# Optimization experiments

Hardware: AMD Instinct MI355X
Metric: run time of the kernel (lower is better)

## Reference

```python
import jax, jax.numpy as jnp
import numpy as np

B, S, H, NH, PF, L = 2, 2048, 1024, 16, 4096, 6
HD = H // NH
EPS = 1e-5


def setup_inputs() -> dict:
    key = jax.random.key(0)
    ks = jax.random.split(key, 12)
    s = lambda k, shp, fan: jax.random.normal(k, shp, jnp.float32) * (1.0 / np.sqrt(fan))
    return {
        "input_tensor": jax.random.normal(ks[0], (B, S, H), jnp.float32),
        "pos_emb": s(ks[1], (S, H), H),
        "Wq": s(ks[2], (L, H, H), H), "bq": jnp.zeros((L, H), jnp.float32),
        "Wk": s(ks[3], (L, H, H), H), "bk": jnp.zeros((L, H), jnp.float32),
        "Wv": s(ks[4], (L, H, H), H), "bv": jnp.zeros((L, H), jnp.float32),
        "Wo": s(ks[5], (L, H, H), H), "bo": jnp.zeros((L, H), jnp.float32),
        "ln_g": jnp.ones((L, H), jnp.float32), "ln_b": jnp.zeros((L, H), jnp.float32),
        "W1": s(ks[6], (L, H, PF), H), "b1": jnp.zeros((L, PF), jnp.float32),
        "W2": s(ks[7], (L, PF, H), PF), "b2": jnp.zeros((L, H), jnp.float32),
    }


def _layernorm(x, g, b):
    mu = jnp.mean(x, axis=-1, keepdims=True)
    var = jnp.mean(jnp.square(x - mu), axis=-1, keepdims=True)
    return (x - mu) * jax.lax.rsqrt(var + EPS) * g + b


def _encoder(input_tensor, pos_emb, params):
    # pos embed: same positions for every batch row
    src = input_tensor * jnp.sqrt(jnp.float32(H)) + pos_emb[None, :, :]

    def layer(src, p):
        Wq, bq, Wk, bk, Wv, bv, Wo, bo, g, b, W1, b1, W2, b2 = p
        q = (src @ Wq + bq).reshape(B, S, NH, HD)
        k = (src @ Wk + bk).reshape(B, S, NH, HD)
        v = (src @ Wv + bv).reshape(B, S, NH, HD)
        # scores [B, NH, S, S]
        energy = jnp.einsum("bqhd,bkhd->bhqk", q, k) / jnp.sqrt(jnp.float32(HD))
        attn = jax.nn.softmax(energy, axis=-1)
        ctx = jnp.einsum("bhqk,bkhd->bqhd", attn, v).reshape(B, S, H)
        attn_out = ctx @ Wo + bo
        src = _layernorm(src + attn_out, g, b)
        ffn = jax.nn.relu(src @ W1 + b1) @ W2 + b2
        src = _layernorm(src + ffn, g, b)  # same LayerNorm reused, as in source
        return src, None

    src, _ = jax.lax.scan(layer, src, params)
    return src


def reference(input_tensor, pos_emb, Wq, bq, Wk, bk, Wv, bv, Wo, bo, ln_g, ln_b, W1, b1, W2, b2):
    params = (Wq, bq, Wk, bk, Wv, bv, Wo, bo, ln_g, ln_b, W1, b1, W2, b2)
    return _encoder(input_tensor, pos_emb, params)
```

## Files before the change

kernel.cpp:

```cpp
#include <hip/hip_runtime.h>
#include <cstdint>

constexpr int Bc = 2, Sc = 2048, Hc = 1024, NHc = 16, HDc = 64, PFc = 4096, Lc = 6;
constexpr float EPSc = 1e-5f;
constexpr float QSC = 0.18033688011112042f;

using f32x4  = __attribute__((ext_vector_type(4))) float;
using bf16x8 = __attribute__((ext_vector_type(8))) __bf16;
using bf16x4 = __attribute__((ext_vector_type(4))) __bf16;
using u32x4  = __attribute__((ext_vector_type(4))) unsigned;

#if __has_builtin(__builtin_amdgcn_exp2f)
#define EXP2(x) __builtin_amdgcn_exp2f(x)
#else
#define EXP2(x) exp2f(x)
#endif

__device__ __forceinline__ f32x4 mfma16(bf16x8 a, bf16x8 b, f32x4 c) {
    return __builtin_amdgcn_mfma_f32_16x16x32_bf16(a, b, c, 0, 0, 0);
}

__device__ __forceinline__ void gload_lds16(const void* g, void* l) {
    __builtin_amdgcn_global_load_lds(
        (__attribute__((address_space(1))) void*)(uintptr_t)g,
        (__attribute__((address_space(3))) void*)(uint32_t)(uintptr_t)l,
        16, 0, 0);
}

struct HL { __bf16 h, l; };
__device__ __forceinline__ HL split2(float v) {
    HL r;
    r.h = (__bf16)v;
    r.l = (__bf16)(v - (float)r.h);
    return r;
}

__device__ __forceinline__ unsigned bfbits(__bf16 x) {
    return (unsigned)__builtin_bit_cast(unsigned short, x);
}
__device__ __forceinline__ unsigned packbf(float a, float b) {
    return bfbits((__bf16)a) | (bfbits((__bf16)b) << 16);
}

__global__ __launch_bounds__(256) void wconv_kernel(
    const float* __restrict__ in, __bf16* __restrict__ out, int K, int N)
{
    __shared__ float tile[64][65];
    const int t = threadIdx.x;
    const size_t lstride = (size_t)K * N;
    const float* ip = in + (size_t)blockIdx.z * lstride;
    __bf16* op = out + (size_t)blockIdx.z * lstride;
    const int n0 = blockIdx.x * 64, k0 = blockIdx.y * 64;
    #pragma unroll
    for (int c = 0; c < 4; ++c) {
        int idx = c * 256 + t;
        int row = idx >> 4;
        int c4  = idx & 15;
        float4 v = *(const float4*)(ip + (size_t)(k0 + row) * N + n0 + c4 * 4);
        tile[row][c4 * 4 + 0] = v.x; tile[row][c4 * 4 + 1] = v.y;
        tile[row][c4 * 4 + 2] = v.z; tile[row][c4 * 4 + 3] = v.w;
    }
    __syncthreads();
    #pragma unroll
    for (int c = 0; c < 4; ++c) {
        int idx = c * 256 + t;
        int n  = idx >> 4;
        int k4 = idx & 15;
        bf16x4 hh = { (__bf16)tile[k4 * 4 + 0][n], (__bf16)tile[k4 * 4 + 1][n],
                      (__bf16)tile[k4 * 4 + 2][n], (__bf16)tile[k4 * 4 + 3][n] };
        *(bf16x4*)(op + (size_t)(n0 + n) * K + k0 + k4 * 4) = hh;
    }
}

__global__ __launch_bounds__(256) void embed_kernel(
    const float* __restrict__ in, const float* __restrict__ pos,
    float* __restrict__ sf, __bf16* __restrict__ sh, __bf16* __restrict__ sl)
{
    const int n4 = (Bc * Sc * Hc) / 4;
    const int pmask = (Sc * Hc / 4) - 1;
    for (int i = blockIdx.x * 256 + threadIdx.x; i < n4; i += gridDim.x * 256) {
        float4 a = ((const float4*)in)[i];
        float4 p = ((const float4*)pos)[i & pmask];
        float4 r;
        r.x = a.x * 32.f + p.x; r.y = a.y * 32.f + p.y;
        r.z = a.z * 32.f + p.z; r.w = a.w * 32.f + p.w;
        ((float4*)sf)[i] = r;
        HL e0 = split2(r.x), e1 = split2(r.y), e2 = split2(r.z), e3 = split2(r.w);
        bf16x4 hh = { e0.h, e1.h, e2.h, e3.h };
        bf16x4 ll = { e0.l, e1.l, e2.l, e3.l };
        ((bf16x4*)sh)[i] = hh;
        ((bf16x4*)sl)[i] = ll;
    }
}

template<int BM, int OUTMODE, bool RELU>
__global__ __launch_bounds__(256) void gemm_bt_kernel(
    const __bf16* __restrict__ A, const __bf16* __restrict__ Wt,
    const float* __restrict__ bias, void* __restrict__ out,
    int M, int N, int K)
{
    constexpr int MI = BM / 32;
    __shared__ alignas(16) __bf16 Alds[BM * 64];
    __shared__ alignas(16) __bf16 Blds[128 * 64];

    const int tid = threadIdx.x, lane = tid & 63, wave = tid >> 6;
    const int lr = lane & 15, lg = lane >> 4;
    const int m0 = blockIdx.y * BM, n0 = blockIdx.x * 128;
    const int wm = (wave >> 1) * (BM / 2), wn = (wave & 1) * 64;

    f32x4 acc[MI][4] = {};

    for (int k0 = 0; k0 < K; k0 += 64) {
        #pragma unroll
        for (int c = 0; c < BM / 32; ++c) {
            int li = c * 256 + tid;
            int row = li >> 3;
            int lcb = ((li & 7) << 4) ^ ((row & 7) << 4);
            gload_lds16(A + (size_t)(m0 + row) * K + k0 + (lcb >> 1),
                        (char*)Alds + (size_t)(c * 256 + wave * 64) * 16);
        }
        #pragma unroll
        for (int c = 0; c < 4; ++c) {
            int li = c * 256 + tid;
            int row = li >> 3;
            int lcb = ((li & 7) << 4) ^ ((row & 7) << 4);
            gload_lds16(Wt + (size_t)(n0 + row) * K + k0 + (lcb >> 1),
                        (char*)Blds + (size_t)(c * 256 + wave * 64) * 16);
        }
        __syncthreads();

        bf16x8 af[2][MI], bfr[2][4];
        #pragma unroll
        for (int ks = 0; ks < 2; ++ks) {
            #pragma unroll
            for (int i = 0; i < MI; ++i) {
                int ra = wm + i * 16 + lr;
                int pa = (ks * 64 + lg * 16) ^ ((ra & 7) << 4);
                af[ks][i] = *(const bf16x8*)((const char*)Alds + ra * 128 + pa);
            }
            #pragma unroll
            for (int i = 0; i < 4; ++i) {
                int rb = wn + i * 16 + lr;
                int pb = (ks * 64 + lg * 16) ^ ((rb & 7) << 4);
                bfr[ks][i] = *(const bf16x8*)((const char*)Blds + rb * 128 + pb);
            }
        }
        #pragma unroll
        for (int ks = 0; ks < 2; ++ks)
            #pragma unroll
            for (int mi = 0; mi < MI; ++mi)
                #pragma unroll
                for (int ni = 0; ni < 4; ++ni)
                    acc[mi][ni] = mfma16(af[ks][mi], bfr[ks][ni], acc[mi][ni]);
        __syncthreads();
    }

    #pragma unroll
    for (int ni = 0; ni < 4; ++ni) {
        int col = n0 + wn + ni * 16 + lr;
        float bv = bias[col];
        #pragma unroll
        for (int mi = 0; mi < MI; ++mi) {
            int rowb = m0 + wm + mi * 16 + lg * 4;
            #pragma unroll
            for (int r = 0; r < 4; ++r) {
                float v = acc[mi][ni][r] + bv;
                if (RELU) v = fmaxf(v, 0.f);
                size_t idx = (size_t)(rowb + r) * N + col;
                if constexpr (OUTMODE == 0) ((float*)out)[idx] = v;
                else                        ((__bf16*)out)[idx] = (__bf16)v;
            }
        }
    }
}

struct QKVBT {
    const __bf16 *wq, *wk, *wv;
    const float *bq, *bk, *bv;
    __bf16 *q, *k, *v;
};

__global__ __launch_bounds__(256) void qkv_bt_kernel(
    const __bf16* __restrict__ A, QKVBT a)
{
    constexpr int N = Hc, K = Hc;
    __shared__ alignas(16) __bf16 Alds[128 * 64];
    __shared__ alignas(16) __bf16 Blds[128 * 64];

    const int tid = threadIdx.x, lane = tid & 63, wave = tid >> 6;
    const int lr = lane & 15, lg = lane >> 4;
    const int gx = blockIdx.x;
    const int widx = gx >> 3;
    const int n0 = (gx & 7) * 128;
    const int m0 = blockIdx.y * 128;
    const int wm = (wave >> 1) * 64, wn = (wave & 1) * 64;

    const __bf16* Wt  = (widx == 0) ? a.wq : (widx == 1) ? a.wk : a.wv;
    const float* bias = (widx == 0) ? a.bq : (widx == 1) ? a.bk : a.bv;

    f32x4 acc[4][4] = {};

    for (int k0 = 0; k0 < K; k0 += 64) {
        #pragma unroll
        for (int c = 0; c < 4; ++c) {
            int li = c * 256 + tid;
            int row = li >> 3;
            int lcb = ((li & 7) << 4) ^ ((row & 7) << 4);
            gload_lds16(A + (size_t)(m0 + row) * K + k0 + (lcb >> 1),
                        (char*)Alds + (size_t)(c * 256 + wave * 64) * 16);
            gload_lds16(Wt + (size_t)(n0 + row) * K + k0 + (lcb >> 1),
                        (char*)Blds + (size_t)(c * 256 + wave * 64) * 16);
        }
        __syncthreads();

        bf16x8 af[2][4], bfr[2][4];
        #pragma unroll
        for (int ks = 0; ks < 2; ++ks) {
            #pragma unroll
            for (int i = 0; i < 4; ++i) {
                int ra = wm + i * 16 + lr;
                int pa = (ks * 64 + lg * 16) ^ ((ra & 7) << 4);
                af[ks][i] = *(const bf16x8*)((const char*)Alds + ra * 128 + pa);
                int rb = wn + i * 16 + lr;
                int pb = (ks * 64 + lg * 16) ^ ((rb & 7) << 4);
                bfr[ks][i] = *(const bf16x8*)((const char*)Blds + rb * 128 + pb);
            }
        }
        #pragma unroll
        for (int ks = 0; ks < 2; ++ks)
            #pragma unroll
            for (int mi = 0; mi < 4; ++mi)
                #pragma unroll
                for (int ni = 0; ni < 4; ++ni)
                    acc[mi][ni] = mfma16(af[ks][mi], bfr[ks][ni], acc[mi][ni]);
        __syncthreads();
    }

    __bf16* outp = (widx == 0) ? a.q : (widx == 1) ? a.k : a.v;
    const float osc = (widx == 0) ? QSC : 1.f;
    #pragma unroll
    for (int ni = 0; ni < 4; ++ni) {
        int col = n0 + wn + ni * 16 + lr;
        float bv = bias[col];
        int hh = col >> 6, d = col & 63;
        #pragma unroll
        for (int mi = 0; mi < 4; ++mi) {
            int rowb = m0 + wm + mi * 16 + lg * 4;
            #pragma unroll
            for (int r = 0; r < 4; ++r) {
                int row = rowb + r;
                int bb = row >> 11, s = row & (Sc - 1);
                outp[((size_t)(bb * NHc + hh) * Sc + s) * HDc + d] =
                    (__bf16)((acc[mi][ni][r] + bv) * osc);
            }
        }
    }
}

struct QKVArgs {
    const float *Wq, *Wk, *Wv, *bq, *bk, *bv;
    __bf16 *qh, *ql, *kh, *kl, *vv;
};

__global__ __launch_bounds__(256) void qkv0_kernel(
    const __bf16* __restrict__ Ahi, const __bf16* __restrict__ Alo, QKVArgs a)
{
    constexpr int N = Hc, K = Hc;
    __shared__ alignas(16) __bf16 AldsH[128 * 64];
    __shared__ alignas(16) __bf16 AldsL[128 * 64];
    __shared__ alignas(16) __bf16 BldsH[128 * 64];
    __shared__ alignas(16) __bf16 BldsL[128 * 64];

    const int tid  = threadIdx.x;
    const int lane = tid & 63;
    const int wave = tid >> 6;
    const int lr   = lane & 15;
    const int lg   = lane >> 4;
    const int gx   = blockIdx.x;
    const int widx = gx >> 3;
    const int n0   = (gx & 7) * 128;
    const int m0   = blockIdx.y * 128;
    const int wm   = (wave >> 1) * 64;
    const int wn   = (wave & 1) * 64;
    const int bn   = tid & 127;
    const int bkh  = (tid >> 7) * 32;

    const float* Bw   = (widx == 0) ? a.Wq : (widx == 1) ? a.Wk : a.Wv;
    const float* bias = (widx == 0) ? a.bq : (widx == 1) ? a.bk : a.bv;

    f32x4 acc[4][4] = {};
    const float* bsrc0 = Bw + (size_t)bkh * N + n0 + bn;

    for (int k0 = 0; k0 < K; k0 += 64) {
        #pragma unroll
        for (int c = 0; c < 4; ++c) {
            int li  = c * 256 + tid;
            int row = li >> 3;
            int lcb = ((li & 7) << 4) ^ ((row & 7) << 4);
            size_t goff = (size_t)(m0 + row) * K + k0 + (lcb >> 1);
            size_t loff = (size_t)(c * 256 + wave * 64) * 16;
            gload_lds16(Ahi + goff, (char*)AldsH + loff);
            gload_lds16(Alo + goff, (char*)AldsL + loff);
        }
        const float* bs = bsrc0 + (size_t)k0 * N;
        #pragma unroll
        for (int c = 0; c < 4; ++c) {
            bf16x8 ph, plv;
            #pragma unroll
            for (int j = 0; j < 8; ++j) {
                HL e = split2(bs[(size_t)(c * 8 + j) * N]);
                ph[j] = e.h;
                plv[j] = e.l;
            }
            int pcb = (bkh * 2 + c * 16) ^ ((bn & 7) << 4);
            *(bf16x8*)((char*)BldsH + bn * 128 + pcb) = ph;
            *(bf16x8*)((char*)BldsL + bn * 128 + pcb) = plv;
        }
        __syncthreads();

        bf16x8 ah[2][4], al[2][4], bh[2][4], bl[2][4];
        #pragma unroll
        for (int ks = 0; ks < 2; ++ks) {
            #pragma unroll
            for (int i = 0; i < 4; ++i) {
                int ra = wm + i * 16 + lr;
                int pa = (ks * 64 + lg * 16) ^ ((ra & 7) << 4);
                ah[ks][i] = *(const bf16x8*)((const char*)AldsH + ra * 128 + pa);
                al[ks][i] = *(const bf16x8*)((const char*)AldsL + ra * 128 + pa);
                int rb = wn + i * 16 + lr;
                int pb = (ks * 64 + lg * 16) ^ ((rb & 7) << 4);
                bh[ks][i] = *(const bf16x8*)((const char*)BldsH + rb * 128 + pb);
                bl[ks][i] = *(const bf16x8*)((const char*)BldsL + rb * 128 + pb);
            }
        }
        #pragma unroll
        for (int ks = 0; ks < 2; ++ks)
            #pragma unroll
            for (int mi = 0; mi < 4; ++mi)
                #pragma unroll
                for (int ni = 0; ni < 4; ++ni) {
                    acc[mi][ni] = mfma16(ah[ks][mi], bh[ks][ni], acc[mi][ni]);
                    acc[mi][ni] = mfma16(al[ks][mi], bh[ks][ni], acc[mi][ni]);
                    acc[mi][ni] = mfma16(ah[ks][mi], bl[ks][ni], acc[mi][ni]);
                }
        __syncthreads();
    }

    __bf16* outh = (widx == 0) ? a.qh : (widx == 1) ? a.kh : a.vv;
    __bf16* outl = (widx == 0) ? a.ql : a.kl;
    const float osc = (widx == 0) ? QSC : 1.f;
    #pragma unroll
    for (int ni = 0; ni < 4; ++ni) {
        int col = n0 + wn + ni * 16 + lr;
        float bv = bias[col];
        int hh = col >> 6, d = col & 63;
        #pragma unroll
        for (int mi = 0; mi < 4; ++mi) {
            int rowb = m0 + wm + mi * 16 + lg * 4;
            #pragma unroll
            for (int r = 0; r < 4; ++r) {
                int row = rowb + r;
                int bb = row >> 11, s = row & (Sc - 1);
                size_t idx = ((size_t)(bb * NHc + hh) * Sc + s) * HDc + d;
                float v = (acc[mi][ni][r] + bv) * osc;
                if (widx < 2) {
                    HL e = split2(v);
                    outh[idx] = e.h;
                    outl[idx] = e.l;
                } else {
                    outh[idx] = (__bf16)v;
                }
            }
        }
    }
}

template<int QKSPLIT>
__global__ __launch_bounds__(256) void attn_kernel(
    const __bf16* __restrict__ Qh, const __bf16* __restrict__ Ql,
    const __bf16* __restrict__ Kh, const __bf16* __restrict__ Kl,
    const __bf16* __restrict__ V, __bf16* __restrict__ O)
{
    __shared__ alignas(16) __bf16 Ksh[2][64 * 64];
    __shared__ alignas(16) __bf16 Klo[QKSPLIT ? 2 : 1][QKSPLIT ? 64 * 64 : 8];
    __shared__ alignas(16) __bf16 VT[2][64 * 64];

    const int tid = threadIdx.x;
    const int lane = tid & 63, wave = tid >> 6;
    const int lr = lane & 15, lg = lane >> 4;
    const int h = blockIdx.y, b = blockIdx.z;
    const int q0 = blockIdx.x * 64 + wave * 16;

    const size_t headoff = ((size_t)b * NHc + h) * Sc * HDc;
    const __bf16* Qb  = Qh + headoff;
    const __bf16* Kb  = Kh + headoff;
    const __bf16* Klb = QKSPLIT ? (Kl + headoff) : nullptr;
    const __bf16* Vb  = V + headoff;

    const size_t qrow = (size_t)(q0 + lr) * HDc;
    bf16x8 qf0 = *(const bf16x8*)(Qb + qrow + lg * 8);
    bf16x8 qf1 = *(const bf16x8*)(Qb + qrow + 32 + lg * 8);
    bf16x8 qlo0, qlo1;
    if constexpr (QKSPLIT) {
        const __bf16* Qlb = Ql + headoff;
        qlo0 = *(const bf16x8*)(Qlb + qrow + lg * 8);
        qlo1 = *(const bf16x8*)(Qlb + qrow + 32 + lg * 8);
    }

    const int kp = tid & 31, dblk = tid >> 5;
    const int sp = (kp & 0x11) | ((kp & 0x06) << 1) | ((kp & 0x08) >> 2);

    auto stageK = [&](int kt, int buf) {
        #pragma unroll
        for (int c = 0; c < 2; ++c) {
            int li  = c * 256 + tid;
            int row = li >> 3;
            int lcb = ((li & 7) << 4) ^ ((row & 7) << 4);
            size_t goff = (size_t)(kt * 64 + row) * HDc + (lcb >> 1);
            size_t loff = (size_t)(c * 256 + wave * 64) * 16;
            gload_lds16(Kb + goff, (char*)Ksh[buf] + loff);
            if constexpr (QKSPLIT)
                gload_lds16(Klb + goff, (char*)Klo[buf] + loff);
        }
    };
    auto loadV = [&](int kt, bf16x8& va, bf16x8& vb2) {
        const __bf16* vs = Vb + (size_t)(kt * 64 + 2 * kp) * HDc + dblk * 8;
        va  = *(const bf16x8*)vs;
        vb2 = *(const bf16x8*)(vs + HDc);
    };
    auto writeVT = [&](int buf, bf16x8 va, bf16x8 vb2) {
        #pragma unroll
        for (int j = 0; j < 8; ++j) {
            int d = dblk * 8 + j;
            unsigned u = bfbits(va[j]) | (bfbits(vb2[j]) << 16);
            int byte = d * 128 + ((sp * 4) ^ ((d & 7) << 4));
            *(unsigned*)((char*)VT[buf] + byte) = u;
        }
    };

    f32x4 o[4] = {};
    float m = -1e30f, lsum = 0.f;

    stageK(0, 0);
    {
        bf16x8 va, vb2;
        loadV(0, va, vb2);
        writeVT(0, va, vb2);
    }
    __syncthreads();

    int cur = 0;
    for (int kt = 0; kt < Sc / 64; ++kt) {
        const int nb = cur ^ 1;
        const bool pf = (kt + 1 < Sc / 64);
        bf16x8 va, vb2;
        if (pf) {
            stageK(kt + 1, nb);
            loadV(kt + 1, va, vb2);
        }

        const char* Kc = (const char*)Ksh[cur];
        const char* Klc = (const char*)Klo[QKSPLIT ? cur : 0];
        f32x4 s[4];
        #pragma unroll
        for (int kg = 0; kg < 4; ++kg) {
            int ra = kg * 16 + lr;
            int pa0 = (lg * 16) ^ ((ra & 7) << 4);
            int pa1 = (64 + lg * 16) ^ ((ra & 7) << 4);
            bf16x8 kf0 = *(const bf16x8*)(Kc + ra * 128 + pa0);
            bf16x8 kf1 = *(const bf16x8*)(Kc + ra * 128 + pa1);
            f32x4 t = {};
            t = mfma16(kf0, qf0, t);
            t = mfma16(kf1, qf1, t);
            if constexpr (QKSPLIT) {
                bf16x8 kg0 = *(const bf16x8*)(Klc + ra * 128 + pa0);
                bf16x8 kg1 = *(const bf16x8*)(Klc + ra * 128 + pa1);
                t = mfma16(kg0, qf0, t);
                t = mfma16(kg1, qf1, t);
                t = mfma16(kf0, qlo0, t);
                t = mfma16(kf1, qlo1, t);
            }
            s[kg] = t;
        }

        float mt = -1e30f;
        #pragma unroll
        for (int kg = 0; kg < 4; ++kg)
            #pragma unroll
            for (int r = 0; r < 4; ++r)
                mt = fmaxf(mt, s[kg][r]);
        mt = fmaxf(mt, __shfl_xor(mt, 16));
        mt = fmaxf(mt, __shfl_xor(mt, 32));
        if (!__all(mt <= m + 8.f)) {
            float mnew = fmaxf(m, mt);
            float fac = EXP2(m - mnew);
            m = mnew;
            lsum *= fac;
            #pragma unroll
            for (int r = 0; r < 4; ++r) {
                float fr = __shfl(fac, (lg << 4) | (lg * 4 + r));
                #pragma unroll
                for (int nd = 0; nd < 4; ++nd) o[nd][r] *= fr;
            }
        }
        float ps = 0.f;
        #pragma unroll
        for (int kg = 0; kg < 4; ++kg)
            #pragma unroll
            for (int r = 0; r < 4; ++r) {
                float p = EXP2(s[kg][r] - m);
                ps += p;
                s[kg][r] = p;
            }
        ps += __shfl_xor(ps, 16);
        ps += __shfl_xor(ps, 32);
        lsum += ps;

        #pragma unroll
        for (int kh2 = 0; kh2 < 2; ++kh2) {
            u32x4 pk;
            pk[0] = packbf(s[2 * kh2][0],     s[2 * kh2][1]);
            pk[1] = packbf(s[2 * kh2][2],     s[2 * kh2][3]);
            pk[2] = packbf(s[2 * kh2 + 1][0], s[2 * kh2 + 1][1]);
            pk[3] = packbf(s[2 * kh2 + 1][2], s[2 * kh2 + 1][3]);
            bf16x8 paf = __builtin_bit_cast(bf16x8, pk);
            #pragma unroll
            for (int nd = 0; nd < 4; ++nd) {
                int d = nd * 16 + lr;
                int byte = d * 128 + ((64 * kh2 + 16 * lg) ^ ((d & 7) << 4));
                bf16x8 vbf = *(const bf16x8*)((const char*)VT[cur] + byte);
                o[nd] = mfma16(paf, vbf, o[nd]);
            }
        }

        if (pf) writeVT(nb, va, vb2);
        __syncthreads();
        cur = nb;
    }

    #pragma unroll
    for (int r = 0; r < 4; ++r) {
        float lv  = __shfl(lsum, (lg << 4) | (lg * 4 + r));
        float inv = 1.f / lv;
        size_t orow = ((size_t)b * Sc + q0 + lg * 4 + r) * Hc + h * HDc;
        #pragma unroll
        for (int nd = 0; nd < 4; ++nd)
            O[orow + nd * 16 + lr] = (__bf16)(o[nd][r] * inv);
    }
}

__global__ __launch_bounds__(256) void ln_kernel(
    const float* __restrict__ xr, const __bf16* __restrict__ y,
    const float* __restrict__ g, const float* __restrict__ beta,
    float* __restrict__ of, __bf16* __restrict__ oh)
{
    __shared__ float red[2][4];
    const int row = blockIdx.x, t = threadIdx.x;
    const int lane = t & 63, wave = t >> 6;
    const int idx = row * 256 + t;
    float4 a = ((const float4*)xr)[idx];
    bf16x4 cb = ((const bf16x4*)y)[idx];
    float4 v;
    v.x = a.x + (float)cb[0]; v.y = a.y + (float)cb[1];
    v.z = a.z + (float)cb[2]; v.w = a.w + (float)cb[3];
    float s1 = v.x + v.y + v.z + v.w;
    float s2 = v.x * v.x + v.y * v.y + v.z * v.z + v.w * v.w;
    #pragma unroll
    for (int off = 1; off < 64; off <<= 1) {
        s1 += __shfl_xor(s1, off);
        s2 += __shfl_xor(s2, off);
    }
    if (lane == 0) { red[0][wave] = s1; red[1][wave] = s2; }
    __syncthreads();
    s1 = red[0][0] + red[0][1] + red[0][2] + red[0][3];
    s2 = red[1][0] + red[1][1] + red[1][2] + red[1][3];
    const float mu   = s1 * (1.f / Hc);
    const float var  = s2 * (1.f / Hc) - mu * mu;
    const float rstd = rsqrtf(var + EPSc);
    float4 gg = ((const float4*)g)[t];
    float4 bb = ((const float4*)beta)[t];
    float4 r;
    r.x = (v.x - mu) * rstd * gg.x + bb.x;
    r.y = (v.y - mu) * rstd * gg.y + bb.y;
    r.z = (v.z - mu) * rstd * gg.z + bb.z;
    r.w = (v.w - mu) * rstd * gg.w + bb.w;
    ((float4*)of)[idx] = r;
    bf16x4 hh = { (__bf16)r.x, (__bf16)r.y, (__bf16)r.z, (__bf16)r.w };
    ((bf16x4*)oh)[idx] = hh;
}

extern "C" void kernel_launch(void* const* d_in, const int* in_sizes, int n_in,
                              void* d_out, int out_size, void* d_ws, size_t ws_size,
                              hipStream_t stream)
{
    const float* inp = (const float*)d_in[0];
    const float* pos = (const float*)d_in[1];
    const float* Wq  = (const float*)d_in[2];
    const float* bq  = (const float*)d_in[3];
    const float* Wk  = (const float*)d_in[4];
    const float* bk  = (const float*)d_in[5];
    const float* Wv  = (const float*)d_in[6];
    const float* bv  = (const float*)d_in[7];
    const float* Wo  = (const float*)d_in[8];
    const float* bo  = (const float*)d_in[9];
    const float* lng = (const float*)d_in[10];
    const float* lnb = (const float*)d_in[11];
    const float* W1  = (const float*)d_in[12];
    const float* b1  = (const float*)d_in[13];
    const float* W2  = (const float*)d_in[14];
    const float* b2  = (const float*)d_in[15];

    char* ws = (char*)d_ws;
    const size_t MB = 1u << 20;
    float*  src_f = (float*)(ws);
    __bf16* src_h = (__bf16*)(ws + 16 * MB);
    __bf16* src_l = (__bf16*)(ws + 24 * MB);
    __bf16* qh    = (__bf16*)(ws + 32 * MB);
    __bf16* kh    = (__bf16*)(ws + 40 * MB);
    __bf16* vv    = (__bf16*)(ws + 48 * MB);
    __bf16* ctx   = (__bf16*)(ws + 56 * MB);
    __bf16* ql    = (__bf16*)(ws + 64 * MB);
    __bf16* kl    = (__bf16*)(ws + 72 * MB);
    __bf16* tmpb  = (__bf16*)(ws + 80 * MB);
    __bf16* h1    = (__bf16*)(ws + 32 * MB);
    __bf16* wqT   = (__bf16*)(ws + 96 * MB);
    __bf16* wkT   = (__bf16*)(ws + 108 * MB);
    __bf16* wvT   = (__bf16*)(ws + 120 * MB);
    __bf16* woT   = (__bf16*)(ws + 132 * MB);
    __bf16* w1T   = (__bf16*)(ws + 144 * MB);
    __bf16* w2T   = (__bf16*)(ws + 192 * MB);

    const int M = Bc * Sc;

    wconv_kernel<<<dim3(16, 16, 6), 256, 0, stream>>>(Wq, wqT, Hc, Hc);
    wconv_kernel<<<dim3(16, 16, 6), 256, 0, stream>>>(Wk, wkT, Hc, Hc);
    wconv_kernel<<<dim3(16, 16, 6), 256, 0, stream>>>(Wv, wvT, Hc, Hc);
    wconv_kernel<<<dim3(16, 16, 6), 256, 0, stream>>>(Wo, woT, Hc, Hc);
    wconv_kernel<<<dim3(64, 16, 6), 256, 0, stream>>>(W1, w1T, Hc, PFc);
    wconv_kernel<<<dim3(16, 64, 6), 256, 0, stream>>>(W2, w2T, PFc, Hc);

    embed_kernel<<<2048, 256, 0, stream>>>(inp, pos, src_f, src_h, src_l);

    for (int l = 0; l < Lc; ++l) {
        const size_t wHH = (size_t)l * Hc * Hc;
        const size_t wH  = (size_t)l * Hc;
        if (l == 0) {
            QKVArgs qa = { Wq, Wk, Wv, bq, bk, bv, qh, ql, kh, kl, vv };
            qkv0_kernel<<<dim3(24, 32), 256, 0, stream>>>(src_h, src_l, qa);
            attn_kernel<1><<<dim3(32, 16, 2), 256, 0, stream>>>(qh, ql, kh, kl, vv, ctx);
        } else {
            QKVBT qa = { wqT + wHH, wkT + wHH, wvT + wHH, bq + wH, bk + wH, bv + wH,
                         qh, kh, vv };
            qkv_bt_kernel<<<dim3(24, 32), 256, 0, stream>>>(src_h, qa);
            attn_kernel<0><<<dim3(32, 16, 2), 256, 0, stream>>>(qh, nullptr, kh, nullptr, vv, ctx);
        }
        gemm_bt_kernel<64, 1, false><<<dim3(8, 64), 256, 0, stream>>>(
            ctx, woT + wHH, bo + wH, tmpb, M, Hc, Hc);
        ln_kernel<<<M, 256, 0, stream>>>(src_f, tmpb, lng + wH, lnb + wH, src_f, src_h);
        gemm_bt_kernel<128, 1, true><<<dim3(32, 32), 256, 0, stream>>>(
            src_h, w1T + (size_t)l * Hc * PFc, b1 + (size_t)l * PFc, h1, M, PFc, Hc);
        gemm_bt_kernel<64, 1, false><<<dim3(8, 64), 256, 0, stream>>>(
            h1, w2T + (size_t)l * PFc * Hc, b2 + wH, tmpb, M, Hc, PFc);
        float* dst = (l == Lc - 1) ? (float*)d_out : src_f;
        ln_kernel<<<M, 256, 0, stream>>>(src_f, tmpb, lng + wH, lnb + wH, dst, src_h);
    }
}
```

Measured before the change: 1.832 ms.

## Double-buffer LDS tiles in GEMM and QKV kernels to overlap loads with MFMA

```diff
diff --git a/kernel.cpp b/kernel.cpp
--- a/kernel.cpp
+++ b/kernel.cpp
@@ -100,8 +100,8 @@
     int M, int N, int K)
 {
     constexpr int MI = BM / 32;
-    __shared__ alignas(16) __bf16 Alds[BM * 64];
-    __shared__ alignas(16) __bf16 Blds[128 * 64];
+    __shared__ alignas(16) __bf16 Alds[2][BM * 64];
+    __shared__ alignas(16) __bf16 Blds[2][128 * 64];
 
     const int tid = threadIdx.x, lane = tid & 63, wave = tid >> 6;
     const int lr = lane & 15, lg = lane >> 4;
@@ -110,14 +110,14 @@
 
     f32x4 acc[MI][4] = {};
 
-    for (int k0 = 0; k0 < K; k0 += 64) {
+    auto stage = [&](int k0, int buf) {
         #pragma unroll
         for (int c = 0; c < BM / 32; ++c) {
             int li = c * 256 + tid;
             int row = li >> 3;
             int lcb = ((li & 7) << 4) ^ ((row & 7) << 4);
             gload_lds16(A + (size_t)(m0 + row) * K + k0 + (lcb >> 1),
-                        (char*)Alds + (size_t)(c * 256 + wave * 64) * 16);
+                        (char*)Alds[buf] + (size_t)(c * 256 + wave * 64) * 16);
         }
         #pragma unroll
         for (int c = 0; c < 4; ++c) {
@@ -125,9 +125,16 @@
             int row = li >> 3;
             int lcb = ((li & 7) << 4) ^ ((row & 7) << 4);
             gload_lds16(Wt + (size_t)(n0 + row) * K + k0 + (lcb >> 1),
-                        (char*)Blds + (size_t)(c * 256 + wave * 64) * 16);
-        }
-        __syncthreads();
+                        (char*)Blds[buf] + (size_t)(c * 256 + wave * 64) * 16);
+        }
+    };
+
+    stage(0, 0);
+    __syncthreads();
+    int cur = 0;
+
+    for (int k0 = 0; k0 < K; k0 += 64) {
+        if (k0 + 64 < K) stage(k0 + 64, cur ^ 1);
 
         bf16x8 af[2][MI], bfr[2][4];
         #pragma unroll
@@ -136,13 +143,13 @@
             for (int i = 0; i < MI; ++i) {
                 int ra = wm + i * 16 + lr;
                 int pa = (ks * 64 + lg * 16) ^ ((ra & 7) << 4);
-                af[ks][i] = *(const bf16x8*)((const char*)Alds + ra * 128 + pa);
+                af[ks][i] = *(const bf16x8*)((const char*)Alds[cur] + ra * 128 + pa);
             }
             #pragma unroll
             for (int i = 0; i < 4; ++i) {
                 int rb = wn + i * 16 + lr;
                 int pb = (ks * 64 + lg * 16) ^ ((rb & 7) << 4);
-                bfr[ks][i] = *(const bf16x8*)((const char*)Blds + rb * 128 + pb);
+                bfr[ks][i] = *(const bf16x8*)((const char*)Blds[cur] + rb * 128 + pb);
             }
         }
         #pragma unroll
@@ -152,7 +159,9 @@
                 #pragma unroll
                 for (int ni = 0; ni < 4; ++ni)
                     acc[mi][ni] = mfma16(af[ks][mi], bfr[ks][ni], acc[mi][ni]);
+
         __syncthreads();
+        cur ^= 1;
     }
 
     #pragma unroll
@@ -184,8 +193,8 @@
     const __bf16* __restrict__ A, QKVBT a)
 {
     constexpr int N = Hc, K = Hc;
-    __shared__ alignas(16) __bf16 Alds[128 * 64];
-    __shared__ alignas(16) __bf16 Blds[128 * 64];
+    __shared__ alignas(16) __bf16 Alds[2][128 * 64];
+    __shared__ alignas(16) __bf16 Blds[2][128 * 64];
 
     const int tid = threadIdx.x, lane = tid & 63, wave = tid >> 6;
     const int lr = lane & 15, lg = lane >> 4;
@@ -200,18 +209,25 @@
 
     f32x4 acc[4][4] = {};
 
-    for (int k0 = 0; k0 < K; k0 += 64) {
+    auto stage = [&](int k0, int buf) {
         #pragma unroll
         for (int c = 0; c < 4; ++c) {
             int li = c * 256 + tid;
             int row = li >> 3;
             int lcb = ((li & 7) << 4) ^ ((row & 7) << 4);
             gload_lds16(A + (size_t)(m0 + row) * K + k0 + (lcb >> 1),
-                        (char*)Alds + (size_t)(c * 256 + wave * 64) * 16);
+                        (char*)Alds[buf] + (size_t)(c * 256 + wave * 64) * 16);
             gload_lds16(Wt + (size_t)(n0 + row) * K + k0 + (lcb >> 1),
-                        (char*)Blds + (size_t)(c * 256 + wave * 64) * 16);
-        }
-        __syncthreads();
+                        (char*)Blds[buf] + (size_t)(c * 256 + wave * 64) * 16);
+        }
+    };
+
+    stage(0, 0);
+    __syncthreads();
+    int cur = 0;
+
+    for (int k0 = 0; k0 < K; k0 += 64) {
+        if (k0 + 64 < K) stage(k0 + 64, cur ^ 1);
 
         bf16x8 af[2][4], bfr[2][4];
         #pragma unroll
@@ -220,10 +236,10 @@
             for (int i = 0; i < 4; ++i) {
                 int ra = wm + i * 16 + lr;
                 int pa = (ks * 64 + lg * 16) ^ ((ra & 7) << 4);
-                af[ks][i] = *(const bf16x8*)((const char*)Alds + ra * 128 + pa);
+                af[ks][i] = *(const bf16x8*)((const char*)Alds[cur] + ra * 128 + pa);
                 int rb = wn + i * 16 + lr;
                 int pb = (ks * 64 + lg * 16) ^ ((rb & 7) << 4);
-                bfr[ks][i] = *(const bf16x8*)((const char*)Blds + rb * 128 + pb);
+                bfr[ks][i] = *(const bf16x8*)((const char*)Blds[cur] + rb * 128 + pb);
             }
         }
         #pragma unroll
@@ -233,7 +249,9 @@
                 #pragma unroll
                 for (int ni = 0; ni < 4; ++ni)
                     acc[mi][ni] = mfma16(af[ks][mi], bfr[ks][ni], acc[mi][ni]);
+
         __syncthreads();
+        cur ^= 1;
     }
 
     __bf16* outp = (widx == 0) ? a.q : (widx == 1) ? a.k : a.v;
```

After: 1.707 ms. 6.8% less time.
